# Kernel tuning notes

Hardware: AMD Instinct MI355X
Metric: run time of the kernel (lower is better)

Reference implementation:

```python
import jax, jax.numpy as jnp
import numpy as np

B, T, D, H = 4, 2048, 1024, 16
HD = D // H  # head_dim = 64


def setup_inputs() -> dict:
    key = jax.random.key(0)
    k1, k2, k3, k4, k5 = jax.random.split(key, 5)
    scale = 1.0 / np.sqrt(D)
    return {
        "x": jax.random.normal(k1, (B, T, D), dtype=jnp.float32),
        "mask": jnp.ones((B, T), dtype=jnp.int32),
        "W_qkv": jax.random.normal(k2, (D, 3 * D), dtype=jnp.float32) * scale,
        "b_qkv": jax.random.normal(k3, (3 * D,), dtype=jnp.float32) * 0.01,
        "W_out": jax.random.normal(k4, (D, D), dtype=jnp.float32) * scale,
        "b_out": jax.random.normal(k5, (D,), dtype=jnp.float32) * 0.01,
    }


def reference(x, mask, W_qkv, b_qkv, W_out, b_out):
    Bx, Tx, Dm = x.shape
    qkv = x @ W_qkv + b_qkv                      # [B,T,3D]
    qkv = qkv.reshape(Bx, Tx, 3, H, HD)
    qkv = jnp.transpose(qkv, (2, 0, 3, 1, 4))    # [3,B,H,T,hd]
    q, k, v = qkv[0], qkv[1], qkv[2]
    att = jnp.einsum("bhqd,bhkd->bhqk", q, k) / jnp.sqrt(jnp.float32(HD))
    m = (mask[:, None, None, :] == 0)            # [B,1,1,T]
    att = jnp.where(m, jnp.float32(-1e9), att)
    att = jax.nn.softmax(att, axis=-1)
    out = jnp.einsum("bhqk,bhkd->bhqd", att, v)  # [B,H,T,hd]
    out = jnp.transpose(out, (0, 2, 1, 3)).reshape(Bx, Tx, Dm)
    return out @ W_out + b_out
```

## Files before the change

### kernel.cpp

```cpp
#include <hip/hip_runtime.h>
#include <hip/hip_bf16.h>
#include <stdint.h>

#define B_  4
#define T_  2048
#define D_  1024
#define H_  16
#define HD_ 64

typedef short s16x8 __attribute__((ext_vector_type(8)));
typedef short s16x4 __attribute__((ext_vector_type(4)));
typedef float f32x4 __attribute__((ext_vector_type(4)));

#define MFMA32(a, b, c) __builtin_amdgcn_mfma_f32_16x16x32_bf16(a, b, c, 0, 0, 0)

#if __has_builtin(__builtin_amdgcn_exp2f)
#define FEXP2(x) __builtin_amdgcn_exp2f(x)
#else
#define FEXP2(x) exp2f(x)
#endif

__device__ __forceinline__ unsigned short f2bf(float f) {
    union { float f; unsigned int u; } v; v.f = f;
    unsigned int r = v.u + 0x7fffu + ((v.u >> 16) & 1u);
    return (unsigned short)(r >> 16);
}

__device__ __forceinline__ unsigned int pkbf(float a, float b) {
    __hip_bfloat162 h = __float22bfloat162_rn(float2{a, b});
    union { __hip_bfloat162 h; unsigned int u; } v; v.h = h;
    return v.u;
}

__device__ __forceinline__ void async16(const void* g, void* l) {
    __builtin_amdgcn_global_load_lds(
        (const __attribute__((address_space(1))) unsigned int*)g,
        (__attribute__((address_space(3))) unsigned int*)l, 16, 0, 0);
}

__global__ __launch_bounds__(256)
void prep_kernel(const float* __restrict__ x, unsigned short* __restrict__ xb,
                 const float* __restrict__ Wq, unsigned short* __restrict__ Wqt,
                 const float* __restrict__ Wo, unsigned short* __restrict__ Wot) {
    const int blk = blockIdx.x;
    const int tid = threadIdx.x;
    if (blk < 8192) {
        const int i = blk * 256 + tid;
        float4 v = ((const float4*)x)[i];
        ushort4 o;
        o.x = f2bf(v.x); o.y = f2bf(v.y); o.z = f2bf(v.z); o.w = f2bf(v.w);
        ((ushort4*)xb)[i] = o;
        return;
    }
    __shared__ float t[32][33];
    const float* W; unsigned short* Wt; int K, N, bx, by;
    if (blk < 11264) {
        const int idx = blk - 8192;
        W = Wq; Wt = Wqt; K = 1024; N = 3072;
        bx = (idx % 96) * 32; by = (idx / 96) * 32;
    } else {
        const int idx = blk - 11264;
        W = Wo; Wt = Wot; K = 1024; N = 1024;
        bx = (idx % 32) * 32; by = (idx / 32) * 32;
    }
    const int tx = tid & 31, ty = tid >> 5;
    #pragma unroll
    for (int j = 0; j < 32; j += 8)
        t[ty + j][tx] = W[(size_t)(by + ty + j) * N + bx + tx];
    __syncthreads();
    #pragma unroll
    for (int j = 0; j < 32; j += 8)
        Wt[(size_t)(bx + ty + j) * K + by + tx] = f2bf(t[tx][ty + j]);
}

template <int MODE>
__global__ __launch_bounds__(256)
void gemm_bt_kernel(const unsigned short* __restrict__ A,
                    const unsigned short* __restrict__ Bt,
                    const float* __restrict__ bias,
                    float* __restrict__ Cf,
                    unsigned short* __restrict__ Qo,
                    unsigned short* __restrict__ Ko,
                    unsigned short* __restrict__ Vo,
                    int M, int N, int K) {
    __shared__ __align__(16) unsigned short SMEM[4 * 128 * 64];
    const int tid = threadIdx.x;
    const int w = tid >> 6, lane = tid & 63;
    const int laneN = lane & 15, quad = lane >> 4;
    const int rm0 = blockIdx.x * 128;
    const int rn0 = blockIdx.y * 128;
    const int wr = (w >> 1) * 64, wc = (w & 1) * 64;

    f32x4 acc[4][4] = {};

    auto issueG = [&](int kk, int bufsel) {
        unsigned short* As = SMEM + bufsel * 8192;
        unsigned short* Bs = SMEM + 16384 + bufsel * 8192;
        #pragma unroll
        for (int i = 0; i < 4; ++i) {
            const int c = i * 256 + tid;
            const int row = c >> 3, s = c & 7, g = s ^ (row & 7);
            async16(A + (size_t)(rm0 + row) * K + kk + g * 8,
                    (char*)As + (size_t)c * 16);
        }
        #pragma unroll
        for (int i = 0; i < 4; ++i) {
            const int c = i * 256 + tid;
            const int row = c >> 3, s = c & 7, g = s ^ (row & 7);
            async16(Bt + (size_t)(rn0 + row) * K + kk + g * 8,
                    (char*)Bs + (size_t)c * 16);
        }
    };

    issueG(0, 0);
    const int KI = K >> 6;
    for (int it = 0; it < KI; ++it) {
        const int buf = it & 1;
        __syncthreads();
        const unsigned short* As = SMEM + buf * 8192;
        const unsigned short* Bs = SMEM + 16384 + buf * 8192;
        s16x8 av[2][4], bv[2][4];
        #pragma unroll
        for (int h = 0; h < 2; ++h) {
            #pragma unroll
            for (int ms = 0; ms < 4; ++ms) {
                const int row = wr + ms * 16 + laneN;
                av[h][ms] = *(const s16x8*)&As[row * 64 + ((h * 4 + quad) ^ (row & 7)) * 8];
            }
            #pragma unroll
            for (int ns = 0; ns < 4; ++ns) {
                const int row = wc + ns * 16 + laneN;
                bv[h][ns] = *(const s16x8*)&Bs[row * 64 + ((h * 4 + quad) ^ (row & 7)) * 8];
            }
        }
        if (it + 1 < KI) issueG((it + 1) << 6, buf ^ 1);
        #pragma unroll
        for (int ms = 0; ms < 4; ++ms)
            #pragma unroll
            for (int ns = 0; ns < 4; ++ns) {
                acc[ms][ns] = MFMA32(av[0][ms], bv[0][ns], acc[ms][ns]);
                acc[ms][ns] = MFMA32(av[1][ms], bv[1][ns], acc[ms][ns]);
            }
    }

    if (MODE == 0) {
        #pragma unroll
        for (int ms = 0; ms < 4; ++ms) {
            const int gm0 = rm0 + wr + ms * 16 + quad * 4;
            #pragma unroll
            for (int ns = 0; ns < 4; ++ns) {
                const int gn = rn0 + wc + ns * 16 + laneN;
                const float bb = bias[gn];
                #pragma unroll
                for (int r = 0; r < 4; ++r)
                    Cf[(size_t)(gm0 + r) * N + gn] = acc[ms][ns][r] + bb;
            }
        }
    }
}

__global__ __launch_bounds__(512, 2)
void gemm256_qkv_kernel(const unsigned short* __restrict__ A,
                        const unsigned short* __restrict__ Bt,
                        const float* __restrict__ bias,
                        unsigned short* __restrict__ Qo,
                        unsigned short* __restrict__ Ko,
                        unsigned short* __restrict__ Vo,
                        int M, int N, int K) {
    __shared__ __align__(16) unsigned short SMEM[65536];
    const int tid = threadIdx.x;
    const int w = tid >> 6, lane = tid & 63;
    const int laneN = lane & 15, quad = lane >> 4;
    const int wm = w >> 2, wn = w & 3;
    const int rm0 = blockIdx.x * 256;
    const int rn0 = blockIdx.y * 256;

    f32x4 acc[8][4] = {};

    auto issueTile = [&](int kk, int bufsel) {
        unsigned short* As = SMEM + bufsel * 16384;
        unsigned short* Bs = SMEM + 32768 + bufsel * 16384;
        #pragma unroll
        for (int i = 0; i < 4; ++i) {
            const int c = i * 512 + tid;
            const int row = c >> 3, s = c & 7, g = s ^ (row & 7);
            async16(A + (size_t)(rm0 + row) * K + kk + g * 8,
                    (char*)As + (size_t)c * 16);
        }
        #pragma unroll
        for (int i = 0; i < 4; ++i) {
            const int c = i * 512 + tid;
            const int row = c >> 3, s = c & 7, g = s ^ (row & 7);
            async16(Bt + (size_t)(rn0 + row) * K + kk + g * 8,
                    (char*)Bs + (size_t)c * 16);
        }
    };

    issueTile(0, 0);
    issueTile(64, 1);
    asm volatile("s_waitcnt vmcnt(8)" ::: "memory");
    __builtin_amdgcn_s_barrier();
    asm volatile("" ::: "memory");

    const int KI = K >> 6;
    #pragma unroll 2
    for (int kt = 0; kt < KI; ++kt) {
        const int buf = kt & 1;
        const unsigned short* As = SMEM + buf * 16384;
        const unsigned short* Bs = SMEM + 32768 + buf * 16384;
        s16x8 av[4], bv[4];
        #pragma unroll
        for (int kh = 0; kh < 2; ++kh) {
            #pragma unroll
            for (int ns = 0; ns < 4; ++ns) {
                const int row = wn * 64 + ns * 16 + laneN;
                bv[ns] = *(const s16x8*)&Bs[row * 64 + ((kh * 4 + quad) ^ (row & 7)) * 8];
            }
            #pragma unroll
            for (int ms = 0; ms < 4; ++ms) {
                const int row = wm * 128 + ms * 16 + laneN;
                av[ms] = *(const s16x8*)&As[row * 64 + ((kh * 4 + quad) ^ (row & 7)) * 8];
            }
            __builtin_amdgcn_s_setprio(1);
            #pragma unroll
            for (int ms = 0; ms < 4; ++ms)
                #pragma unroll
                for (int ns = 0; ns < 4; ++ns)
                    acc[ms][ns] = MFMA32(av[ms], bv[ns], acc[ms][ns]);
            __builtin_amdgcn_s_setprio(0);
            #pragma unroll
            for (int ms = 0; ms < 4; ++ms) {
                const int row = wm * 128 + 64 + ms * 16 + laneN;
                av[ms] = *(const s16x8*)&As[row * 64 + ((kh * 4 + quad) ^ (row & 7)) * 8];
            }
            __builtin_amdgcn_s_setprio(1);
            #pragma unroll
            for (int ms = 0; ms < 4; ++ms)
                #pragma unroll
                for (int ns = 0; ns < 4; ++ns)
                    acc[4 + ms][ns] = MFMA32(av[ms], bv[ns], acc[4 + ms][ns]);
            __builtin_amdgcn_s_setprio(0);
        }
        __builtin_amdgcn_s_barrier();
        asm volatile("" ::: "memory");
        if (kt + 2 < KI) {
            issueTile((kt + 2) << 6, buf);
            asm volatile("s_waitcnt vmcnt(8)" ::: "memory");
        } else if (kt + 1 < KI) {
            asm volatile("s_waitcnt vmcnt(0)" ::: "memory");
        }
        if (kt + 1 < KI) {
            __builtin_amdgcn_s_barrier();
            asm volatile("" ::: "memory");
        }
    }

    const int s = rn0 >> 10;
    const int bidx = rm0 >> 11, t0 = rm0 & (T_ - 1);
    if (s < 2) {
        const float fs = (s == 0) ? 0.125f * 1.44269504088896f : 1.0f;
        unsigned short* P = (s == 0) ? Qo : Ko;
        #pragma unroll
        for (int a = 0; a < 8; ++a) {
            const int lm0 = wm * 128 + (a >> 2) * 64 + (a & 3) * 16 + quad * 4;
            #pragma unroll
            for (int ns = 0; ns < 4; ++ns) {
                const int gn = rn0 + wn * 64 + ns * 16 + laneN;
                const float bb = bias[gn];
                const int rr = gn & 1023, hh = rr >> 6, dd = rr & 63;
                const size_t base = ((size_t)(bidx * H_ + hh) * T_ + t0);
                #pragma unroll
                for (int r = 0; r < 4; ++r)
                    P[(base + lm0 + r) * HD_ + dd] =
                        f2bf((acc[a][ns][r] + bb) * fs);
            }
        }
    } else {
        __syncthreads();
        #pragma unroll
        for (int a = 0; a < 8; ++a) {
            const int lm0 = wm * 128 + (a >> 2) * 64 + (a & 3) * 16 + quad * 4;
            #pragma unroll
            for (int ns = 0; ns < 4; ++ns) {
                const int nl = wn * 64 + ns * 16 + laneN;
                const float bb = bias[rn0 + nl];
                const int sw = (nl & 7) << 3;
                #pragma unroll
                for (int r = 0; r < 4; ++r)
                    SMEM[nl * 256 + ((lm0 + r) ^ sw)] =
                        f2bf(acc[a][ns][r] + bb);
            }
        }
        __syncthreads();
        const int nl = tid >> 1, half = tid & 1;
        const int hh = nl >> 6, d = nl & 63;
        const int hAbs = bidx * H_ + ((rn0 & 1023) >> 6) + hh;
        unsigned short* rowp = Vo + ((size_t)hAbs * HD_ + d) * T_ + t0;
        const int swz = nl & 7;
        #pragma unroll
        for (int j = 0; j < 16; ++j) {
            const int mgl = half * 16 + j;
            const int pg = (mgl & 24) | ((mgl & 7) ^ swz);
            const s16x8 vv = *(const s16x8*)&SMEM[nl * 256 + pg * 8];
            *(s16x8*)(rowp + mgl * 8) = vv;
        }
    }
}

__global__ __launch_bounds__(512, 4)
void attn_kernel(const unsigned short* __restrict__ Q,
                 const unsigned short* __restrict__ Kb,
                 const unsigned short* __restrict__ VT,
                 const int* __restrict__ mask,
                 unsigned short* __restrict__ Out) {
    __shared__ __align__(16) unsigned short Ks[2][64 * 64];
    __shared__ __align__(16) unsigned short Vs[2][64 * 64];
    __shared__ float biasF[T_];
    const int tid = threadIdx.x;
    const int lane = tid & 63;
    const int w = tid >> 6;
    const int laneN = lane & 15, quad = lane >> 4;
    const int x7 = laneN & 7;
    const int bh = blockIdx.x;
    const int b = bh >> 4, h = bh & 15;
    const int qbase = blockIdx.y * 256 + w * 32;

    for (int i = tid; i < T_; i += 512)
        biasF[i] = mask[b * T_ + i] ? 0.f : -1.0e9f;

    s16x8 qf[2][2];
    #pragma unroll
    for (int qg = 0; qg < 2; ++qg) {
        const size_t qoff = ((size_t)bh * T_ + qbase + qg * 16 + laneN) * HD_ + quad * 8;
        qf[qg][0] = *(const s16x8*)&Q[qoff];
        qf[qg][1] = *(const s16x8*)&Q[qoff + 32];
    }

    s16x8 ones;
    #pragma unroll
    for (int j = 0; j < 8; ++j) ones[j] = (short)0x3F80;

    const size_t kRow0 = (size_t)bh * T_ * HD_;
    const size_t vRow0 = (size_t)bh * HD_ * T_;

    auto issueTile = [&](int kt, int bufsel) {
        const int kbase = kt * 64;
        {
            const int c = tid;
            const int row = c >> 3, s = c & 7;
            const int fk = (row & 3) | (((row >> 3) & 1) << 2);
            const int g = s ^ fk;
            async16(Kb + kRow0 + (size_t)(kbase + row) * HD_ + g * 8,
                    &Ks[bufsel][c * 8]);
        }
        {
            const int c = tid;
            const int d = c >> 3, s = c & 7, g = s ^ (d & 7);
            async16(VT + vRow0 + (size_t)d * T_ + kbase + g * 8,
                    &Vs[bufsel][c * 8]);
        }
    };

    issueTile(0, 0);

    f32x4 O[2][4] = {};
    f32x4 liacc[2] = {};

    const int rowA = ((laneN >> 2) << 3) + (laneN & 3);

    #pragma unroll 2
    for (int kt = 0; kt < T_ / 64; ++kt) {
        const int buf = kt & 1;
        const int kbase = kt * 64;
        __syncthreads();
        if (kt + 1 < T_ / 64) issueTile(kt + 1, buf ^ 1);

        s16x8 pf[2][2];
        #pragma unroll
        for (int g32 = 0; g32 < 2; ++g32) {
            const int ra = g32 * 32 + rowA;
            const s16x8 kA0 = *(const s16x8*)&Ks[buf][(ra * 8 + (quad ^ x7)) * 8];
            const s16x8 kA1 = *(const s16x8*)&Ks[buf][(ra * 8 + ((4 + quad) ^ x7)) * 8];
            const s16x8 kB0 = *(const s16x8*)&Ks[buf][((ra + 4) * 8 + (quad ^ x7)) * 8];
            const s16x8 kB1 = *(const s16x8*)&Ks[buf][((ra + 4) * 8 + ((4 + quad) ^ x7)) * 8];
            const f32x4 bA = *(const f32x4*)&biasF[kbase + g32 * 32 + quad * 8];
            const f32x4 bB = *(const f32x4*)&biasF[kbase + g32 * 32 + quad * 8 + 4];
            #pragma unroll
            for (int qg = 0; qg < 2; ++qg) {
                f32x4 Sa = bA, Sb = bB;
                Sa = MFMA32(kA0, qf[qg][0], Sa);
                Sa = MFMA32(kA1, qf[qg][1], Sa);
                Sb = MFMA32(kB0, qf[qg][0], Sb);
                Sb = MFMA32(kB1, qf[qg][1], Sb);
                #pragma unroll
                for (int r = 0; r < 4; ++r) {
                    Sa[r] = FEXP2(Sa[r]);
                    Sb[r] = FEXP2(Sb[r]);
                }
                union { s16x8 v; unsigned int u[4]; } pu;
                pu.u[0] = pkbf(Sa[0], Sa[1]);
                pu.u[1] = pkbf(Sa[2], Sa[3]);
                pu.u[2] = pkbf(Sb[0], Sb[1]);
                pu.u[3] = pkbf(Sb[2], Sb[3]);
                pf[qg][g32] = pu.v;
            }
        }

        #pragma unroll
        for (int g32 = 0; g32 < 2; ++g32) {
            s16x8 vf[4];
            #pragma unroll
            for (int nt = 0; nt < 4; ++nt) {
                const int d = nt * 16 + laneN;
                vf[nt] = *(const s16x8*)&Vs[buf][(d * 8 + ((g32 * 4 + quad) ^ x7)) * 8];
            }
            #pragma unroll
            for (int qg = 0; qg < 2; ++qg) {
                #pragma unroll
                for (int nt = 0; nt < 4; ++nt)
                    O[qg][nt] = MFMA32(pf[qg][g32], vf[nt], O[qg][nt]);
                liacc[qg] = MFMA32(pf[qg][g32], ones, liacc[qg]);
            }
        }
    }

    #pragma unroll
    for (int qg = 0; qg < 2; ++qg) {
        #pragma unroll
        for (int r = 0; r < 4; ++r) {
            const float inv = 1.0f / liacc[qg][r];
            const int tq = qbase + qg * 16 + quad * 4 + r;
            #pragma unroll
            for (int nt = 0; nt < 4; ++nt)
                Out[(size_t)(b * T_ + tq) * D_ + h * HD_ + nt * 16 + laneN] =
                    f2bf(O[qg][nt][r] * inv);
        }
    }
}

extern "C" void kernel_launch(void* const* d_in, const int* in_sizes, int n_in,
                              void* d_out, int out_size, void* d_ws, size_t ws_size,
                              hipStream_t stream) {
    const float* x     = (const float*)d_in[0];
    const int*   mask  = (const int*)d_in[1];
    const float* W_qkv = (const float*)d_in[2];
    const float* b_qkv = (const float*)d_in[3];
    const float* W_out = (const float*)d_in[4];
    const float* b_out = (const float*)d_in[5];
    float* out = (float*)d_out;

    unsigned short* ws = (unsigned short*)d_ws;
    const size_t NX = (size_t)B_ * T_ * D_;
    unsigned short* xb  = ws;
    unsigned short* Qb  = xb + NX;
    unsigned short* Kb  = Qb + NX;
    unsigned short* Vtb = Kb + NX;
    unsigned short* Wqt = Vtb + NX;
    unsigned short* Wot = Wqt + (size_t)3 * D_ * D_;
    unsigned short* attn = xb;

    prep_kernel<<<12288, 256, 0, stream>>>(x, xb, W_qkv, Wqt, W_out, Wot);
    gemm256_qkv_kernel<<<dim3(B_ * T_ / 256, 3 * D_ / 256), 512, 0, stream>>>(
        xb, Wqt, b_qkv, Qb, Kb, Vtb, B_ * T_, 3 * D_, D_);
    attn_kernel<<<dim3(B_ * H_, T_ / 256), 512, 0, stream>>>(Qb, Kb, Vtb, mask, attn);
    gemm_bt_kernel<0><<<dim3(B_ * T_ / 128, D_ / 128), 256, 0, stream>>>(
        attn, Wot, b_out, out, nullptr, nullptr, nullptr, B_ * T_, D_, D_);
}
```

Measured before the change: 264.0 us.

## Shrink QKV GEMM tile to 256x128 with triple-buffered LDS pipeline

The QKV projection GEMM moves from 256x256 tiles to 256x128 tiles, which doubles the grid (32x24 blocks) and halves each warp's accumulator set. The LDS pipeline goes from double to triple buffering, with tiles prefetched three steps ahead and wait counts adjusted. The goal is more blocks to fill the CUs, lower register pressure and better hiding of load latency. In exchange, arithmetic intensity per block drops and the A tile is re-read across twice as many column blocks.

```diff
diff --git a/kernel.cpp b/kernel.cpp
--- a/kernel.cpp
+++ b/kernel.cpp
@@ -160,26 +160,27 @@
 }
 
 __global__ __launch_bounds__(512, 2)
-void gemm256_qkv_kernel(const unsigned short* __restrict__ A,
-                        const unsigned short* __restrict__ Bt,
-                        const float* __restrict__ bias,
-                        unsigned short* __restrict__ Qo,
-                        unsigned short* __restrict__ Ko,
-                        unsigned short* __restrict__ Vo,
-                        int M, int N, int K) {
-    __shared__ __align__(16) unsigned short SMEM[65536];
+void gemm256x128_qkv_kernel(const unsigned short* __restrict__ A,
+                            const unsigned short* __restrict__ Bt,
+                            const float* __restrict__ bias,
+                            unsigned short* __restrict__ Qo,
+                            unsigned short* __restrict__ Ko,
+                            unsigned short* __restrict__ Vo,
+                            int M, int N, int K) {
+    __shared__ __align__(16) unsigned short SMEM[3 * 24576];
     const int tid = threadIdx.x;
     const int w = tid >> 6, lane = tid & 63;
     const int laneN = lane & 15, quad = lane >> 4;
-    const int wm = w >> 2, wn = w & 3;
+    const int wm = w >> 1, wn = w & 1;
     const int rm0 = blockIdx.x * 256;
-    const int rn0 = blockIdx.y * 256;
-
-    f32x4 acc[8][4] = {};
-
-    auto issueTile = [&](int kk, int bufsel) {
-        unsigned short* As = SMEM + bufsel * 16384;
-        unsigned short* Bs = SMEM + 32768 + bufsel * 16384;
+    const int rn0 = blockIdx.y * 128;
+
+    f32x4 acc[4][4] = {};
+
+    auto issueTile = [&](int t, int bufsel) {
+        const int kk = t << 6;
+        unsigned short* As = SMEM + bufsel * 24576;
+        unsigned short* Bs = As + 16384;
         #pragma unroll
         for (int i = 0; i < 4; ++i) {
             const int c = i * 512 + tid;
@@ -188,7 +189,7 @@
                     (char*)As + (size_t)c * 16);
         }
         #pragma unroll
-        for (int i = 0; i < 4; ++i) {
+        for (int i = 0; i < 2; ++i) {
             const int c = i * 512 + tid;
             const int row = c >> 3, s = c & 7, g = s ^ (row & 7);
             async16(Bt + (size_t)(rn0 + row) * K + kk + g * 8,
@@ -197,20 +198,20 @@
     };
 
     issueTile(0, 0);
-    issueTile(64, 1);
-    asm volatile("s_waitcnt vmcnt(8)" ::: "memory");
+    issueTile(1, 1);
+    issueTile(2, 2);
+    asm volatile("s_waitcnt vmcnt(12)" ::: "memory");
     __builtin_amdgcn_s_barrier();
     asm volatile("" ::: "memory");
 
     const int KI = K >> 6;
-    #pragma unroll 2
+    int buf = 0;
     for (int kt = 0; kt < KI; ++kt) {
-        const int buf = kt & 1;
-        const unsigned short* As = SMEM + buf * 16384;
-        const unsigned short* Bs = SMEM + 32768 + buf * 16384;
-        s16x8 av[4], bv[4];
+        const unsigned short* As = SMEM + buf * 24576;
+        const unsigned short* Bs = As + 16384;
         #pragma unroll
         for (int kh = 0; kh < 2; ++kh) {
+            s16x8 av[4], bv[4];
             #pragma unroll
             for (int ns = 0; ns < 4; ++ns) {
                 const int row = wn * 64 + ns * 16 + laneN;
@@ -218,7 +219,7 @@
             }
             #pragma unroll
             for (int ms = 0; ms < 4; ++ms) {
-                const int row = wm * 128 + ms * 16 + laneN;
+                const int row = wm * 64 + ms * 16 + laneN;
                 av[ms] = *(const s16x8*)&As[row * 64 + ((kh * 4 + quad) ^ (row & 7)) * 8];
             }
             __builtin_amdgcn_s_setprio(1);
@@ -228,31 +229,22 @@
                 for (int ns = 0; ns < 4; ++ns)
                     acc[ms][ns] = MFMA32(av[ms], bv[ns], acc[ms][ns]);
             __builtin_amdgcn_s_setprio(0);
-            #pragma unroll
-            for (int ms = 0; ms < 4; ++ms) {
-                const int row = wm * 128 + 64 + ms * 16 + laneN;
-                av[ms] = *(const s16x8*)&As[row * 64 + ((kh * 4 + quad) ^ (row & 7)) * 8];
-            }
-            __builtin_amdgcn_s_setprio(1);
-            #pragma unroll
-            for (int ms = 0; ms < 4; ++ms)
-                #pragma unroll
-                for (int ns = 0; ns < 4; ++ns)
-                    acc[4 + ms][ns] = MFMA32(av[ms], bv[ns], acc[4 + ms][ns]);
-            __builtin_amdgcn_s_setprio(0);
-        }
-        __builtin_amdgcn_s_barrier();
-        asm volatile("" ::: "memory");
-        if (kt + 2 < KI) {
-            issueTile((kt + 2) << 6, buf);
-            asm volatile("s_waitcnt vmcnt(8)" ::: "memory");
-        } else if (kt + 1 < KI) {
-            asm volatile("s_waitcnt vmcnt(0)" ::: "memory");
         }
         if (kt + 1 < KI) {
             __builtin_amdgcn_s_barrier();
             asm volatile("" ::: "memory");
-        }
+            if (kt + 3 < KI) {
+                issueTile(kt + 3, buf);
+                asm volatile("s_waitcnt vmcnt(12)" ::: "memory");
+            } else if (kt + 2 < KI) {
+                asm volatile("s_waitcnt vmcnt(6)" ::: "memory");
+            } else {
+                asm volatile("s_waitcnt vmcnt(0)" ::: "memory");
+            }
+            __builtin_amdgcn_s_barrier();
+            asm volatile("" ::: "memory");
+        }
+        buf = (buf == 2) ? 0 : buf + 1;
     }
 
     const int s = rn0 >> 10;
@@ -261,8 +253,8 @@
         const float fs = (s == 0) ? 0.125f * 1.44269504088896f : 1.0f;
         unsigned short* P = (s == 0) ? Qo : Ko;
         #pragma unroll
-        for (int a = 0; a < 8; ++a) {
-            const int lm0 = wm * 128 + (a >> 2) * 64 + (a & 3) * 16 + quad * 4;
+        for (int ms = 0; ms < 4; ++ms) {
+            const int lm0 = wm * 64 + ms * 16 + quad * 4;
             #pragma unroll
             for (int ns = 0; ns < 4; ++ns) {
                 const int gn = rn0 + wn * 64 + ns * 16 + laneN;
@@ -272,14 +264,14 @@
                 #pragma unroll
                 for (int r = 0; r < 4; ++r)
                     P[(base + lm0 + r) * HD_ + dd] =
-                        f2bf((acc[a][ns][r] + bb) * fs);
+                        f2bf((acc[ms][ns][r] + bb) * fs);
             }
         }
     } else {
         __syncthreads();
         #pragma unroll
-        for (int a = 0; a < 8; ++a) {
-            const int lm0 = wm * 128 + (a >> 2) * 64 + (a & 3) * 16 + quad * 4;
+        for (int ms = 0; ms < 4; ++ms) {
+            const int lm0 = wm * 64 + ms * 16 + quad * 4;
             #pragma unroll
             for (int ns = 0; ns < 4; ++ns) {
                 const int nl = wn * 64 + ns * 16 + laneN;
@@ -288,18 +280,18 @@
                 #pragma unroll
                 for (int r = 0; r < 4; ++r)
                     SMEM[nl * 256 + ((lm0 + r) ^ sw)] =
-                        f2bf(acc[a][ns][r] + bb);
+                        f2bf(acc[ms][ns][r] + bb);
             }
         }
         __syncthreads();
-        const int nl = tid >> 1, half = tid & 1;
+        const int nl = tid >> 2, part = tid & 3;
         const int hh = nl >> 6, d = nl & 63;
         const int hAbs = bidx * H_ + ((rn0 & 1023) >> 6) + hh;
         unsigned short* rowp = Vo + ((size_t)hAbs * HD_ + d) * T_ + t0;
         const int swz = nl & 7;
         #pragma unroll
-        for (int j = 0; j < 16; ++j) {
-            const int mgl = half * 16 + j;
+        for (int j = 0; j < 8; ++j) {
+            const int mgl = part * 8 + j;
             const int pg = (mgl & 24) | ((mgl & 7) ^ swz);
             const s16x8 vv = *(const s16x8*)&SMEM[nl * 256 + pg * 8];
             *(s16x8*)(rowp + mgl * 8) = vv;
@@ -460,7 +452,7 @@
     unsigned short* attn = xb;
 
     prep_kernel<<<12288, 256, 0, stream>>>(x, xb, W_qkv, Wqt, W_out, Wot);
-    gemm256_qkv_kernel<<<dim3(B_ * T_ / 256, 3 * D_ / 256), 512, 0, stream>>>(
+    gemm256x128_qkv_kernel<<<dim3(B_ * T_ / 256, 3 * D_ / 128), 512, 0, stream>>>(
         xb, Wqt, b_qkv, Qb, Kb, Vtb, B_ * T_, 3 * D_, D_);
     attn_kernel<<<dim3(B_ * H_, T_ / 256), 512, 0, stream>>>(Qb, Kb, Vtb, mask, attn);
     gemm_bt_kernel<0><<<dim3(B_ * T_ / 128, D_ / 128), 256, 0, stream>>>(
```

New measurement: 266.2 us. About the same (+0.8%).
